# Optimization experiments

Measured on AMD Instinct MI355X. Metric: run time of the kernel, lower is better.

The kernel has to match this reference:

```python
import jax, jax.numpy as jnp
import numpy as np

B, C_IN, H, W = 32, 12, 495, 436
C_HID = 16


def setup_inputs() -> dict:
    key = jax.random.key(0)
    k_x, k1, k2, k3, kb1, kb2, kb3 = jax.random.split(key, 7)
    x = jax.random.uniform(k_x, (B, C_IN, H, W), dtype=jnp.float32) * 255.0
    # Kaiming-uniform-ish init; exact distribution irrelevant for a correctness baseline.
    def u(k, shape, fan_in):
        bound = 1.0 / np.sqrt(fan_in)
        return jax.random.uniform(k, shape, dtype=jnp.float32, minval=-bound, maxval=bound)
    w1 = u(k1, (C_HID, C_IN), C_IN)   # conv1 1x1 kernel [out, in]
    b1 = u(kb1, (C_HID,), C_IN)
    w2 = u(k2, (C_HID, C_HID), C_HID)
    b2 = u(kb2, (C_HID,), C_HID)
    w3 = u(k3, (1, C_HID), C_HID)
    b3 = u(kb3, (1,), C_HID)
    return {"x": x, "w1": w1, "b1": b1, "w2": w2, "b2": b2, "w3": w3, "b3": b3}


def _conv1x1(x, w, b):
    # x: [B, Cin, H, W], w: [Cout, Cin], b: [Cout]
    return jnp.einsum("bchw,oc->bohw", x, w) + b[None, :, None, None]


def reference(x, w1, b1, w2, b2, w3, b3):
    h = x / 255.0 - 0.5
    h = jax.nn.relu(_conv1x1(h, w1, b1))
    h = jax.nn.relu(_conv1x1(h, w2, b2))
    h = jax.nn.sigmoid(_conv1x1(h, w3, b3))
    return 255.0 * h
```

## Files before the change

kernel.cpp:

```cpp
#include <hip/hip_runtime.h>
#include <math.h>

#define B_    32
#define C_IN  12
#define C_HID 16
#define H_    495
#define W_    436
#define HW    (H_ * W_)
#define NPIX  (B_ * HW)
#define NG2   (NPIX / 2)

__global__ __launch_bounds__(256) void temporal_mlp_kernel(
    const float* __restrict__ x,
    const float* __restrict__ w1, const float* __restrict__ b1,
    const float* __restrict__ w2, const float* __restrict__ b2,
    const float* __restrict__ w3, const float* __restrict__ b3,
    float* __restrict__ out)
{
    const int g = blockIdx.x * 256 + threadIdx.x;
    if (g >= NG2) return;

    const int base = g * 2;
    const int b    = base / HW;
    const int p    = base - b * HW;
    const float* xb = x + (size_t)b * (C_IN * HW) + p;

    float xn0[12], xn1[12];
    #pragma unroll
    for (int c = 0; c < 12; ++c) {
        float2 t = *(const float2*)(xb + (size_t)c * HW);
        xn0[c] = fmaf(t.x, 1.0f / 255.0f, -0.5f);
        xn1[c] = fmaf(t.y, 1.0f / 255.0f, -0.5f);
    }

    float h10[16], h11[16];
    #pragma unroll
    for (int o = 0; o < 16; ++o) {
        const float bb = b1[o];
        float a0 = bb, a1 = bb;
        #pragma unroll
        for (int c = 0; c < 12; ++c) {
            const float w = w1[o * 12 + c];
            a0 = fmaf(xn0[c], w, a0);
            a1 = fmaf(xn1[c], w, a1);
        }
        h10[o] = fmaxf(a0, 0.0f);
        h11[o] = fmaxf(a1, 0.0f);
    }

    float h20[16], h21[16];
    #pragma unroll
    for (int o = 0; o < 16; ++o) {
        const float bb = b2[o];
        float a0 = bb, a1 = bb;
        #pragma unroll
        for (int c = 0; c < 16; ++c) {
            const float w = w2[o * 16 + c];
            a0 = fmaf(h10[c], w, a0);
            a1 = fmaf(h11[c], w, a1);
        }
        h20[o] = fmaxf(a0, 0.0f);
        h21[o] = fmaxf(a1, 0.0f);
    }

    float t0 = b3[0], t1 = b3[0];
    #pragma unroll
    for (int c = 0; c < 16; ++c) {
        const float w = w3[c];
        t0 = fmaf(h20[c], w, t0);
        t1 = fmaf(h21[c], w, t1);
    }

    float2 r;
    r.x = 255.0f / (1.0f + expf(-t0));
    r.y = 255.0f / (1.0f + expf(-t1));
    *(float2*)(out + base) = r;
}

extern "C" void kernel_launch(void* const* d_in, const int* in_sizes, int n_in,
                              void* d_out, int out_size, void* d_ws, size_t ws_size,
                              hipStream_t stream) {
    const float* x  = (const float*)d_in[0];
    const float* w1 = (const float*)d_in[1];
    const float* b1 = (const float*)d_in[2];
    const float* w2 = (const float*)d_in[3];
    const float* b2 = (const float*)d_in[4];
    const float* w3 = (const float*)d_in[5];
    const float* b3 = (const float*)d_in[6];
    float* out = (float*)d_out;

    const int grid = (NG2 + 255) / 256;
    temporal_mlp_kernel<<<grid, 256, 0, stream>>>(x, w1, b1, w2, b2, w3, b3, out);
}
```

Baseline: 466.8 us.

## Fold input normalization into conv1 weights, stage weights in LDS, use packed FMAs

Folds the x/255-0.5 normalization into the first layer's weights and bias, which removes the per-pixel affine step. Each block stages all weights in shared memory as float4 rows. The MLP arithmetic uses 2-wide vector FMA and max builtins so the compiler can emit packed-math instructions, and the sigmoid uses the fast __expf. The kernel is heavily memory bound (12 float reads per pixel), so the compute savings may matter little, and the per-block LDS staging adds a barrier.

```diff
diff --git a/kernel.cpp b/kernel.cpp
--- a/kernel.cpp
+++ b/kernel.cpp
@@ -10,6 +10,30 @@
 #define NPIX  (B_ * HW)
 #define NG2   (NPIX / 2)
 
+typedef float v2f __attribute__((ext_vector_type(2)));
+
+#if __has_builtin(__builtin_elementwise_fma)
+static __device__ __forceinline__ v2f pk_fma(v2f a, float w, v2f c) {
+    v2f ws = {w, w};
+    return __builtin_elementwise_fma(a, ws, c);
+}
+#else
+static __device__ __forceinline__ v2f pk_fma(v2f a, float w, v2f c) {
+    v2f r; r.x = fmaf(a.x, w, c.x); r.y = fmaf(a.y, w, c.y); return r;
+}
+#endif
+
+#if __has_builtin(__builtin_elementwise_max)
+static __device__ __forceinline__ v2f pk_relu(v2f a) {
+    v2f z = {0.0f, 0.0f};
+    return __builtin_elementwise_max(a, z);
+}
+#else
+static __device__ __forceinline__ v2f pk_relu(v2f a) {
+    v2f r; r.x = fmaxf(a.x, 0.0f); r.y = fmaxf(a.y, 0.0f); return r;
+}
+#endif
+
 __global__ __launch_bounds__(256) void temporal_mlp_kernel(
     const float* __restrict__ x,
     const float* __restrict__ w1, const float* __restrict__ b1,
@@ -17,7 +41,32 @@
     const float* __restrict__ w3, const float* __restrict__ b3,
     float* __restrict__ out)
 {
-    const int g = blockIdx.x * 256 + threadIdx.x;
+    __shared__ __align__(16) float4 sW1[16][3];
+    __shared__ __align__(16) float4 sW2[16][4];
+    __shared__ __align__(16) float4 sW3[4];
+    __shared__ float sB1[16];
+    __shared__ float sB2[16];
+    __shared__ float sB3;
+
+    const int tid = threadIdx.x;
+    {
+        float* pW1 = (float*)sW1;
+        float* pW2 = (float*)sW2;
+        if (tid < 192) pW1[tid] = w1[tid] * (1.0f / 255.0f);
+        pW2[tid] = w2[tid];
+        if (tid < 16) {
+            float s = 0.0f;
+            #pragma unroll
+            for (int c = 0; c < 12; ++c) s += w1[tid * 12 + c];
+            sB1[tid] = b1[tid] - 0.5f * s;
+            sB2[tid] = b2[tid];
+            ((float*)sW3)[tid] = w3[tid];
+        }
+        if (tid == 0) sB3 = b3[0];
+    }
+    __syncthreads();
+
+    const int g = blockIdx.x * 256 + tid;
     if (g >= NG2) return;
 
     const int base = g * 2;
@@ -25,55 +74,69 @@
     const int p    = base - b * HW;
     const float* xb = x + (size_t)b * (C_IN * HW) + p;
 
-    float xn0[12], xn1[12];
+    v2f xn[12];
     #pragma unroll
     for (int c = 0; c < 12; ++c) {
         float2 t = *(const float2*)(xb + (size_t)c * HW);
-        xn0[c] = fmaf(t.x, 1.0f / 255.0f, -0.5f);
-        xn1[c] = fmaf(t.y, 1.0f / 255.0f, -0.5f);
+        v2f v = {t.x, t.y};
+        xn[c] = v;
     }
 
-    float h10[16], h11[16];
+    v2f h1[16];
     #pragma unroll
     for (int o = 0; o < 16; ++o) {
-        const float bb = b1[o];
-        float a0 = bb, a1 = bb;
-        #pragma unroll
-        for (int c = 0; c < 12; ++c) {
-            const float w = w1[o * 12 + c];
-            a0 = fmaf(xn0[c], w, a0);
-            a1 = fmaf(xn1[c], w, a1);
-        }
-        h10[o] = fmaxf(a0, 0.0f);
-        h11[o] = fmaxf(a1, 0.0f);
+        const float4 wa = sW1[o][0];
+        const float4 wb = sW1[o][1];
+        const float4 wc = sW1[o][2];
+        const float bb = sB1[o];
+        v2f a = {bb, bb};
+        a = pk_fma(xn[0],  wa.x, a);  a = pk_fma(xn[1],  wa.y, a);
+        a = pk_fma(xn[2],  wa.z, a);  a = pk_fma(xn[3],  wa.w, a);
+        a = pk_fma(xn[4],  wb.x, a);  a = pk_fma(xn[5],  wb.y, a);
+        a = pk_fma(xn[6],  wb.z, a);  a = pk_fma(xn[7],  wb.w, a);
+        a = pk_fma(xn[8],  wc.x, a);  a = pk_fma(xn[9],  wc.y, a);
+        a = pk_fma(xn[10], wc.z, a);  a = pk_fma(xn[11], wc.w, a);
+        h1[o] = pk_relu(a);
     }
 
-    float h20[16], h21[16];
+    v2f h2[16];
     #pragma unroll
     for (int o = 0; o < 16; ++o) {
-        const float bb = b2[o];
-        float a0 = bb, a1 = bb;
-        #pragma unroll
-        for (int c = 0; c < 16; ++c) {
-            const float w = w2[o * 16 + c];
-            a0 = fmaf(h10[c], w, a0);
-            a1 = fmaf(h11[c], w, a1);
-        }
-        h20[o] = fmaxf(a0, 0.0f);
-        h21[o] = fmaxf(a1, 0.0f);
+        const float4 wa = sW2[o][0];
+        const float4 wb = sW2[o][1];
+        const float4 wc = sW2[o][2];
+        const float4 wd = sW2[o][3];
+        const float bb = sB2[o];
+        v2f a = {bb, bb};
+        a = pk_fma(h1[0],  wa.x, a);  a = pk_fma(h1[1],  wa.y, a);
+        a = pk_fma(h1[2],  wa.z, a);  a = pk_fma(h1[3],  wa.w, a);
+        a = pk_fma(h1[4],  wb.x, a);  a = pk_fma(h1[5],  wb.y, a);
+        a = pk_fma(h1[6],  wb.z, a);  a = pk_fma(h1[7],  wb.w, a);
+        a = pk_fma(h1[8],  wc.x, a);  a = pk_fma(h1[9],  wc.y, a);
+        a = pk_fma(h1[10], wc.z, a);  a = pk_fma(h1[11], wc.w, a);
+        a = pk_fma(h1[12], wd.x, a);  a = pk_fma(h1[13], wd.y, a);
+        a = pk_fma(h1[14], wd.z, a);  a = pk_fma(h1[15], wd.w, a);
+        h2[o] = pk_relu(a);
     }
 
-    float t0 = b3[0], t1 = b3[0];
-    #pragma unroll
-    for (int c = 0; c < 16; ++c) {
-        const float w = w3[c];
-        t0 = fmaf(h20[c], w, t0);
-        t1 = fmaf(h21[c], w, t1);
-    }
+    const float4 ua = sW3[0];
+    const float4 ub = sW3[1];
+    const float4 uc = sW3[2];
+    const float4 ud = sW3[3];
+    const float b3v = sB3;
+    v2f t = {b3v, b3v};
+    t = pk_fma(h2[0],  ua.x, t);  t = pk_fma(h2[1],  ua.y, t);
+    t = pk_fma(h2[2],  ua.z, t);  t = pk_fma(h2[3],  ua.w, t);
+    t = pk_fma(h2[4],  ub.x, t);  t = pk_fma(h2[5],  ub.y, t);
+    t = pk_fma(h2[6],  ub.z, t);  t = pk_fma(h2[7],  ub.w, t);
+    t = pk_fma(h2[8],  uc.x, t);  t = pk_fma(h2[9],  uc.y, t);
+    t = pk_fma(h2[10], uc.z, t);  t = pk_fma(h2[11], uc.w, t);
+    t = pk_fma(h2[12], ud.x, t);  t = pk_fma(h2[13], ud.y, t);
+    t = pk_fma(h2[14], ud.z, t);  t = pk_fma(h2[15], ud.w, t);
 
     float2 r;
-    r.x = 255.0f / (1.0f + expf(-t0));
-    r.y = 255.0f / (1.0f + expf(-t1));
+    r.x = 255.0f / (1.0f + __expf(-t.x));
+    r.y = 255.0f / (1.0f + __expf(-t.y));
     *(float2*)(out + base) = r;
 }
 
```

Result: faster. 448.4 us (-4.0%).
